# Performance work log

Measured on AMD Instinct MI355X. Metric: run time of the kernel, lower is better.

## Reference

```python
import jax, jax.numpy as jnp
import numpy as np

N = 32767      # 2**15 - 1 nodes: complete binary tree, parent(i) = (i-1)//2
IN = 512       # in_channels
H = 256        # hidden_dim
OUT = 1        # output_dim
DEPTH = 15     # number of topological levels (static)


def setup_inputs() -> dict:
    key = jax.random.key(0)
    ks = jax.random.split(key, 8)
    x = jax.random.normal(ks[0], (N, IN), dtype=jnp.float32)
    # complete binary tree edge list: edge_index[0]=child, edge_index[1]=parent
    src = jnp.arange(1, N, dtype=jnp.int32)
    dst = (src - 1) // 2
    edge_index = jnp.stack([src, dst])  # [2, N-1]
    s = 1.0 / np.sqrt(H)  # torch LSTMCell/Linear default uniform init scale
    W_ih = jax.random.uniform(ks[1], (4 * H, IN), minval=-s, maxval=s, dtype=jnp.float32)
    W_hh = jax.random.uniform(ks[2], (4 * H, H), minval=-s, maxval=s, dtype=jnp.float32)
    b_ih = jax.random.uniform(ks[3], (4 * H,), minval=-s, maxval=s, dtype=jnp.float32)
    b_hh = jax.random.uniform(ks[4], (4 * H,), minval=-s, maxval=s, dtype=jnp.float32)
    W_fc = jax.random.uniform(ks[5], (OUT, H), minval=-s, maxval=s, dtype=jnp.float32)
    b_fc = jax.random.uniform(ks[6], (OUT,), minval=-s, maxval=s, dtype=jnp.float32)
    return {"x": x, "edge_index": edge_index, "W_ih": W_ih, "W_hh": W_hh,
            "b_ih": b_ih, "b_hh": b_hh, "W_fc": W_fc, "b_fc": b_fc}


def reference(x, edge_index, W_ih, W_hh, b_ih, b_hh, W_fc, b_fc):
    src, dst = edge_index[0], edge_index[1]
    # children count per parent (matches torch children_count loop)
    cnt = jax.ops.segment_sum(jnp.ones_like(src, dtype=x.dtype), dst, num_segments=N)
    cnt = jnp.maximum(cnt, 1.0)[:, None]  # [N,1]; leaves get zero child state anyway
    h = jnp.zeros((N, H), dtype=x.dtype)
    c = jnp.zeros((N, H), dtype=x.dtype)
    # topological sweep: deepest level first (children processed before parents)
    for d in range(DEPTH - 1, -1, -1):
        lo = 2 ** d - 1
        hi = min(2 ** (d + 1) - 1, N)  # level d node index range (static)
        # mean of already-computed child h/c states, gathered via edge list
        mean_h = jax.ops.segment_sum(h[src], dst, num_segments=N)[lo:hi] / cnt[lo:hi]
        mean_c = jax.ops.segment_sum(c[src], dst, num_segments=N)[lo:hi] / cnt[lo:hi]
        # torch LSTMCell: gates in (i, f, g, o) order
        gates = x[lo:hi] @ W_ih.T + b_ih + mean_h @ W_hh.T + b_hh  # [n_level, 4H]
        i, f, g, o = jnp.split(gates, 4, axis=-1)
        i, f, o = jax.nn.sigmoid(i), jax.nn.sigmoid(f), jax.nn.sigmoid(o)
        g = jnp.tanh(g)
        c_new = f * mean_c + i * g
        h_new = o * jnp.tanh(c_new)
        h = h.at[lo:hi].set(h_new)
        c = c.at[lo:hi].set(c_new)
    pooled = jnp.mean(h, axis=0, keepdims=True)  # [1, H]
    out = pooled @ W_fc.T + b_fc                 # [1, 1]
    return out.squeeze(-1)                       # [1]
```

## Files before the change

### kernel.cpp

```cpp
#include <hip/hip_runtime.h>
#include <hip/hip_cooperative_groups.h>
#include <math.h>

namespace cg = cooperative_groups;


#define N_NODES 32767
#define N_LEAF0 16383
#define IN_C    512
#define H_C     256

typedef __bf16 bf16x8 __attribute__((ext_vector_type(8)));
typedef float  f32x4  __attribute__((ext_vector_type(4)));

__device__ __forceinline__ void gload_lds16(const void* g, void* l) {
    __builtin_amdgcn_global_load_lds(
        (const __attribute__((address_space(1))) unsigned int*)g,
        (__attribute__((address_space(3))) unsigned int*)l,
        16, 0, 0);
}

__device__ __forceinline__ float fast_rcp(float x) { return __builtin_amdgcn_rcpf(x); }
__device__ __forceinline__ float sigm(float x)     { return fast_rcp(1.f + __expf(-x)); }
__device__ __forceinline__ float tanh_fast(float x){ return 2.f * fast_rcp(1.f + __expf(-2.f * x)) - 1.f; }

__global__ __launch_bounds__(256)
void conv_bf16_kernel(const float* __restrict__ src, __bf16* __restrict__ dst, int n8)
{
    const int i = blockIdx.x * 256 + threadIdx.x;
    if (i < n8) {
        const float4* s4 = (const float4*)src;
        const float4 a = s4[2 * i];
        const float4 b = s4[2 * i + 1];
        bf16x8 o;
        o[0] = (__bf16)a.x; o[1] = (__bf16)a.y; o[2] = (__bf16)a.z; o[3] = (__bf16)a.w;
        o[4] = (__bf16)b.x; o[5] = (__bf16)b.y; o[6] = (__bf16)b.z; o[7] = (__bf16)b.w;
        *(bf16x8*)(dst + 8 * i) = o;
    }
}

__global__ __launch_bounds__(256)
void bulk_xw(const float* __restrict__ x,
             const __bf16* __restrict__ wih,
             const float* __restrict__ b_ih,
             const float* __restrict__ b_hh,
             __bf16* __restrict__ hb,
             float* __restrict__ c,
             __bf16* __restrict__ gx)
{
    __shared__ __bf16 As[128 * 64];
    __shared__ __bf16 Bs[128 * 64];

    const int t    = threadIdx.x;
    const int lane = t & 63;
    const int wv   = t >> 6;
    const int wm   = wv >> 1;
    const int wn   = wv & 1;
    const int quad = lane >> 4;
    const int l15  = lane & 15;

    const int i  = blockIdx.x;
    const int cb = (i >> 3) & 7;
    const int mt = (i & 7) | ((i >> 6) << 3);
    const int m0 = mt * 128;

    f32x4 acc[4][4];
#pragma unroll
    for (int mi = 0; mi < 4; ++mi)
#pragma unroll
        for (int ni = 0; ni < 4; ++ni) acc[mi][ni] = (f32x4)0.f;

    for (int k0 = 0; k0 < IN_C; k0 += 64) {
#pragma unroll
        for (int e = 0; e < 4; ++e) {
            const int ch = (wv * 4 + e) * 64 + lane;
            const int nl = ch >> 3;
            const int k8 = (ch & 7) ^ (nl & 7);
            const int q  = (nl >> 4) & 3;
            const int cc = (nl & 15) | ((nl >> 6) << 4);
            const int grow = q * H_C + cb * 32 + cc;
            gload_lds16(wih + (size_t)grow * IN_C + k0 + k8 * 8,
                        (char*)Bs + (wv * 4 + e) * 1024);
        }
        {
            const int row  = t >> 1;
            const int kh   = (t & 1) * 32;
            const int node = min(m0 + row, N_NODES - 1);
            const float4* xs = (const float4*)(x + (size_t)node * IN_C + k0 + kh);
#pragma unroll
            for (int j = 0; j < 4; ++j) {
                const float4 v0 = xs[2 * j], v1 = xs[2 * j + 1];
                bf16x8 o;
                o[0] = (__bf16)v0.x; o[1] = (__bf16)v0.y; o[2] = (__bf16)v0.z; o[3] = (__bf16)v0.w;
                o[4] = (__bf16)v1.x; o[5] = (__bf16)v1.y; o[6] = (__bf16)v1.z; o[7] = (__bf16)v1.w;
                const int cs = ((kh >> 3) + j) ^ (row & 7);
                *(bf16x8*)(As + row * 64 + cs * 8) = o;
            }
        }
        __syncthreads();
#pragma unroll
        for (int ks = 0; ks < 2; ++ks) {
            bf16x8 af[4], bfr[4];
#pragma unroll
            for (int mi = 0; mi < 4; ++mi) {
                const int row = wm * 64 + mi * 16 + l15;
                af[mi] = *(const bf16x8*)(As + row * 64 + (((ks * 4 + quad) ^ (row & 7)) << 3));
            }
#pragma unroll
            for (int ni = 0; ni < 4; ++ni) {
                const int row = wn * 64 + ni * 16 + l15;
                bfr[ni] = *(const bf16x8*)(Bs + row * 64 + (((ks * 4 + quad) ^ (row & 7)) << 3));
            }
#pragma unroll
            for (int mi = 0; mi < 4; ++mi)
#pragma unroll
                for (int ni = 0; ni < 4; ++ni)
                    acc[mi][ni] = __builtin_amdgcn_mfma_f32_16x16x32_bf16(
                        af[mi], bfr[ni], acc[mi][ni], 0, 0, 0);
        }
        __syncthreads();
    }

    const int CH = cb * 32 + wn * 16 + l15;
    float bs[4];
#pragma unroll
    for (int q = 0; q < 4; ++q) bs[q] = b_ih[q * H_C + CH] + b_hh[q * H_C + CH];

#pragma unroll
    for (int mi = 0; mi < 4; ++mi) {
#pragma unroll
        for (int r = 0; r < 4; ++r) {
            const int m = m0 + wm * 64 + mi * 16 + quad * 4 + r;
            if (m >= N_NODES) continue;
            if (m >= N_LEAF0) {
                const float gi = sigm(acc[mi][0][r] + bs[0]);
                const float gf = sigm(acc[mi][1][r] + bs[1]);  (void)gf;
                const float gg = tanh_fast(acc[mi][2][r] + bs[2]);
                const float go = sigm(acc[mi][3][r] + bs[3]);
                const float cn = gi * gg;
                const float hn = go * tanh_fast(cn);
                c[(size_t)m * H_C + CH] = cn;
                hb[(size_t)m * H_C + CH] = (__bf16)hn;
            } else {
#pragma unroll
                for (int q = 0; q < 4; ++q)
                    gx[(size_t)m * 1024 + q * H_C + CH] = (__bf16)acc[mi][q][r];
            }
        }
    }
}

__global__ __launch_bounds__(256)
void level_hw(const __bf16* __restrict__ whh,
              const float* __restrict__ b_ih,
              const float* __restrict__ b_hh,
              const __bf16* __restrict__ gx,
              __bf16* __restrict__ hb,
              float* __restrict__ c,
              int lo, int n)
{
    __shared__ __bf16 As[128 * 32];
    __shared__ __bf16 Bs[128 * 32];

    const int t    = threadIdx.x;
    const int lane = t & 63;
    const int wv   = t >> 6;
    const int wm   = wv >> 1;
    const int wn   = wv & 1;
    const int quad = lane >> 4;
    const int l15  = lane & 15;

    const int i = blockIdx.x;
    int cb, mt;
    if (gridDim.x >= 64) { cb = (i >> 3) & 7; mt = (i & 7) | ((i >> 6) << 3); }
    else                 { cb = i & 7;        mt = i >> 3; }
    const int m0 = mt * 128;

    f32x4 acc[4][4];
#pragma unroll
    for (int mi = 0; mi < 4; ++mi)
#pragma unroll
        for (int ni = 0; ni < 4; ++ni) acc[mi][ni] = (f32x4)0.f;

    for (int k0 = 0; k0 < H_C; k0 += 32) {
#pragma unroll
        for (int e = 0; e < 2; ++e) {
            const int chunk = wv * 2 + e;
            const int nl    = chunk * 16 + (lane >> 2);
            const int q     = (nl >> 4) & 3;
            const int cc    = (nl & 15) + ((nl >> 6) << 4);
            const int grow  = q * H_C + cb * 32 + cc;
            const void* g = (const char*)(whh + grow * H_C + k0) + (lane & 3) * 16;
            gload_lds16(g, (char*)Bs + chunk * 1024);
        }
        {
            const int row  = t >> 1;
            const int kh   = (t & 1) * 16;
            const int node = lo + m0 + row;
            const int k2   = k0 + kh;
            const bf16x8* hl = (const bf16x8*)(hb + (size_t)(2 * node + 1) * H_C + k2);
            const bf16x8* hr = (const bf16x8*)(hb + (size_t)(2 * node + 2) * H_C + k2);
            const bf16x8 a0 = hl[0], a1 = hl[1], b0 = hr[0], b1 = hr[1];
            bf16x8 o0, o1;
#pragma unroll
            for (int j = 0; j < 8; ++j) {
                o0[j] = (__bf16)(0.5f * ((float)a0[j] + (float)b0[j]));
                o1[j] = (__bf16)(0.5f * ((float)a1[j] + (float)b1[j]));
            }
            bf16x8* dst = (bf16x8*)(As + row * 32 + kh);
            dst[0] = o0;
            dst[1] = o1;
        }
        __syncthreads();
        bf16x8 af[4], bfr[4];
#pragma unroll
        for (int mi = 0; mi < 4; ++mi)
            af[mi] = *(const bf16x8*)(As + (wm * 64 + mi * 16 + l15) * 32 + quad * 8);
#pragma unroll
        for (int ni = 0; ni < 4; ++ni)
            bfr[ni] = *(const bf16x8*)(Bs + (wn * 64 + ni * 16 + l15) * 32 + quad * 8);
#pragma unroll
        for (int mi = 0; mi < 4; ++mi)
#pragma unroll
            for (int ni = 0; ni < 4; ++ni)
                acc[mi][ni] = __builtin_amdgcn_mfma_f32_16x16x32_bf16(
                    af[mi], bfr[ni], acc[mi][ni], 0, 0, 0);
        __syncthreads();
    }

    const int CH = cb * 32 + wn * 16 + l15;
    float bs[4];
#pragma unroll
    for (int q = 0; q < 4; ++q) bs[q] = b_ih[q * H_C + CH] + b_hh[q * H_C + CH];

#pragma unroll
    for (int mi = 0; mi < 4; ++mi) {
#pragma unroll
        for (int r = 0; r < 4; ++r) {
            const int m = m0 + wm * 64 + mi * 16 + quad * 4 + r;
            if (m < n) {
                const int node = lo + m;
                const float g0 = acc[mi][0][r] + (float)gx[(size_t)node * 1024 + 0 * H_C + CH] + bs[0];
                const float g1 = acc[mi][1][r] + (float)gx[(size_t)node * 1024 + 1 * H_C + CH] + bs[1];
                const float g2 = acc[mi][2][r] + (float)gx[(size_t)node * 1024 + 2 * H_C + CH] + bs[2];
                const float g3 = acc[mi][3][r] + (float)gx[(size_t)node * 1024 + 3 * H_C + CH] + bs[3];
                const float gi = sigm(g0);
                const float gf = sigm(g1);
                const float gg = tanh_fast(g2);
                const float go = sigm(g3);
                const float mc = 0.5f * (c[(size_t)(2 * node + 1) * H_C + CH] +
                                         c[(size_t)(2 * node + 2) * H_C + CH]);
                const float cn = gf * mc + gi * gg;
                const float hn = go * tanh_fast(cn);
                c[(size_t)node * H_C + CH] = cn;
                hb[(size_t)node * H_C + CH] = (__bf16)hn;
            }
        }
    }
}

__global__ __launch_bounds__(256, 1)
void tail_levels(const __bf16* __restrict__ whh,
                 const float* __restrict__ b_ih,
                 const float* __restrict__ b_hh,
                 const __bf16* __restrict__ gx,
                 __bf16* __restrict__ hb,
                 const float* __restrict__ c)
{
    __shared__ __bf16 Ws[128][264];
    __shared__ __align__(16) char UAG[64 * 264 * 2];
    __shared__ float cl[2][64][33];

    const int t    = threadIdx.x;
    const int cb   = blockIdx.x;
    const int lane = t & 63;
    const int wq   = t >> 6;
    const int quad = lane >> 4;
    const int l15  = lane & 15;

    auto As = (__bf16(*)[264])UAG;
    auto Gs = (float(*)[64][33])UAG;

    {
        const int row = t >> 1;
        const int k0  = (t & 1) * 128;
        const int q   = row >> 5, cc = row & 31;
        const __bf16* src = whh + (size_t)(q * H_C + cb * 32 + cc) * H_C + k0;
#pragma unroll
        for (int j = 0; j < 16; ++j)
            *(bf16x8*)(&Ws[row][k0 + 8 * j]) = *(const bf16x8*)(src + 8 * j);
    }
    const int ecc = t & 31;
    const int erg = t >> 5;
    const int CH  = cb * 32 + ecc;
    float bsq[4];
#pragma unroll
    for (int q = 0; q < 4; ++q) bsq[q] = b_ih[q * H_C + CH] + b_hh[q * H_C + CH];

    cg::grid_group grid = cg::this_grid();

    for (int d = 6; d >= 0; --d) {
        const int n  = 1 << d;
        const int lo = n - 1;
        const int pp = d & 1;
        __syncthreads();
        {
            const int row  = t >> 2;
            const int kb   = (t & 3) * 64;
            const int node = lo + row;
            const bf16x8* hl = (const bf16x8*)(hb + (size_t)(2 * node + 1) * H_C + kb);
            const bf16x8* hr = (const bf16x8*)(hb + (size_t)(2 * node + 2) * H_C + kb);
#pragma unroll
            for (int j = 0; j < 8; ++j) {
                const bf16x8 a = hl[j], b = hr[j];
                bf16x8 o;
#pragma unroll
                for (int e = 0; e < 8; ++e)
                    o[e] = (__bf16)(0.5f * ((float)a[e] + (float)b[e]));
                *(bf16x8*)(&As[row][kb + 8 * j]) = o;
            }
        }
        __syncthreads();
        f32x4 acc[4][2];
#pragma unroll
        for (int mi = 0; mi < 4; ++mi)
#pragma unroll
            for (int ni = 0; ni < 2; ++ni) acc[mi][ni] = (f32x4)0.f;
        for (int kk = 0; kk < 8; ++kk) {
#pragma unroll
            for (int mi = 0; mi < 4; ++mi) {
                const bf16x8 af = *(const bf16x8*)(&As[mi * 16 + l15][kk * 32 + quad * 8]);
#pragma unroll
                for (int ni = 0; ni < 2; ++ni) {
                    const bf16x8 bf_ = *(const bf16x8*)(&Ws[wq * 32 + ni * 16 + l15][kk * 32 + quad * 8]);
                    acc[mi][ni] = __builtin_amdgcn_mfma_f32_16x16x32_bf16(af, bf_, acc[mi][ni], 0, 0, 0);
                }
            }
        }
        __syncthreads();
#pragma unroll
        for (int mi = 0; mi < 4; ++mi)
#pragma unroll
            for (int ni = 0; ni < 2; ++ni)
#pragma unroll
                for (int r = 0; r < 4; ++r)
                    Gs[wq][mi * 16 + quad * 4 + r][ni * 16 + l15] = acc[mi][ni][r];
        __syncthreads();
        for (int r = erg; r < n; r += 8) {
            const int node = lo + r;
            float g[4];
#pragma unroll
            for (int q = 0; q < 4; ++q)
                g[q] = Gs[q][r][ecc] + (float)gx[(size_t)node * 1024 + q * H_C + CH] + bsq[q];
            const float gi = sigm(g[0]);
            const float gf = sigm(g[1]);
            const float gg = tanh_fast(g[2]);
            const float go = sigm(g[3]);
            float mc;
            if (d == 6)
                mc = 0.5f * (c[(size_t)(2 * node + 1) * H_C + CH] +
                             c[(size_t)(2 * node + 2) * H_C + CH]);
            else
                mc = 0.5f * (cl[pp ^ 1][2 * r][ecc] + cl[pp ^ 1][2 * r + 1][ecc]);
            const float cn = gf * mc + gi * gg;
            const float hn = go * tanh_fast(cn);
            cl[pp][r][ecc] = cn;
            hb[(size_t)node * H_C + CH] = (__bf16)hn;
        }
        grid.sync();
    }
}

__global__ __launch_bounds__(256)
void reduce_rows(const __bf16* __restrict__ hb, float* __restrict__ part)
{
    __shared__ float sm[8][256];
    const int t  = threadIdx.x;
    const int b  = blockIdx.x;
    const int rg = t >> 5;
    const int c8 = (t & 31) * 8;
    float s[8];
#pragma unroll
    for (int j = 0; j < 8; ++j) s[j] = 0.f;
    for (int i2 = 0; i2 < 16; ++i2) {
        const int row = b * 128 + i2 * 8 + rg;
        if (row < N_NODES) {
            const bf16x8 v = *(const bf16x8*)(hb + (size_t)row * H_C + c8);
#pragma unroll
            for (int j = 0; j < 8; ++j) s[j] += (float)v[j];
        }
    }
#pragma unroll
    for (int j = 0; j < 8; ++j) sm[rg][c8 + j] = s[j];
    __syncthreads();
    float tot = 0.f;
#pragma unroll
    for (int g = 0; g < 8; ++g) tot += sm[g][t];
    part[b * H_C + t] = tot;
}

__global__ __launch_bounds__(256)
void reduce_final(const float* __restrict__ part,
                  const float* __restrict__ W_fc,
                  const float* __restrict__ b_fc,
                  float* __restrict__ out)
{
    __shared__ float sm[256];
    const int t = threadIdx.x;
    float s = 0.f;
    for (int j = 0; j < 256; ++j) s += part[j * H_C + t];
    s = s * (1.0f / (float)N_NODES) * W_fc[t];
    sm[t] = s;
    __syncthreads();
    for (int st = 128; st > 0; st >>= 1) {
        if (t < st) sm[t] += sm[t + st];
        __syncthreads();
    }
    if (t == 0) out[0] = sm[0] + b_fc[0];
}

extern "C" void kernel_launch(void* const* d_in, const int* in_sizes, int n_in,
                              void* d_out, int out_size, void* d_ws, size_t ws_size,
                              hipStream_t stream)
{
    const float* x    = (const float*)d_in[0];
    const float* W_ih = (const float*)d_in[2];
    const float* W_hh = (const float*)d_in[3];
    const float* b_ih = (const float*)d_in[4];
    const float* b_hh = (const float*)d_in[5];
    const float* W_fc = (const float*)d_in[6];
    const float* b_fc = (const float*)d_in[7];
    float* out = (float*)d_out;

    char* w = (char*)d_ws;
    __bf16* hb   = (__bf16*)w;  w += (size_t)N_NODES * H_C * 2;
    float*  c    = (float*)w;   w += (size_t)N_NODES * H_C * 4;
    __bf16* gx   = (__bf16*)w;  w += (size_t)N_LEAF0 * 1024 * 2;
    __bf16* wihb = (__bf16*)w;  w += (size_t)4 * H_C * IN_C * 2;
    __bf16* whhb = (__bf16*)w;  w += (size_t)4 * H_C * H_C * 2;
    float*  part = (float*)w;

    {
        const int n8i = (4 * H_C * IN_C) / 8;
        conv_bf16_kernel<<<(n8i + 255) / 256, 256, 0, stream>>>(W_ih, wihb, n8i);
        const int n8h = (4 * H_C * H_C) / 8;
        conv_bf16_kernel<<<(n8h + 255) / 256, 256, 0, stream>>>(W_hh, whhb, n8h);
    }

    bulk_xw<<<2048, 256, 0, stream>>>(x, wihb, b_ih, b_hh, hb, c, gx);

    for (int d = 13; d >= 7; --d) {
        const int n  = 1 << d;
        const int lo = n - 1;
        const int nm = (n + 127) / 128;
        level_hw<<<nm * 8, 256, 0, stream>>>(whhb, b_ih, b_hh, gx, hb, c, lo, n);
    }

    {
        const __bf16* a0 = whhb; const float* a1 = b_ih; const float* a2 = b_hh;
        const __bf16* a3 = gx;   __bf16* a4 = hb;        const float* a5 = c;
        void* targs[] = {&a0, &a1, &a2, &a3, &a4, &a5};
        hipError_t e = hipLaunchCooperativeKernel((const void*)tail_levels,
                                                  dim3(8), dim3(256), targs, 0, stream);
        if (e != hipSuccess) {
            for (int d = 6; d >= 0; --d) {
                const int n  = 1 << d;
                const int lo = n - 1;
                level_hw<<<8, 256, 0, stream>>>(whhb, b_ih, b_hh, gx, hb, c, lo, n);
            }
        }
    }

    reduce_rows<<<256, 256, 0, stream>>>(hb, part);
    reduce_final<<<1, 256, 0, stream>>>(part, W_fc, b_fc, out);
}
```

Measured before the change: 422.1 us.

## Fuse pooling into level kernels, merge weight casts, extend cooperative tail to more levels

Several changes at once. The two weight-conversion kernels are merged into one grid-stride launch. The x loads in bulk_xw are register-prefetched one k-step ahead. The gx layout is interleaved so each node/channel reads one 8-byte vector. level_hw gets a larger K tile with a swizzled LDS layout. The mean-pool is fused into every stage through atomic per-channel sums, which removes the two reduction kernels. The cooperative 8-block tail now covers levels 9..0 in 64-row chunks, replacing three more launches but doing more serial work on only 8 blocks.

```diff
diff --git a/kernel.cpp b/kernel.cpp
--- a/kernel.cpp
+++ b/kernel.cpp
@@ -11,6 +11,7 @@
 #define H_C     256
 
 typedef __bf16 bf16x8 __attribute__((ext_vector_type(8)));
+typedef __bf16 bf16x4 __attribute__((ext_vector_type(4)));
 typedef float  f32x4  __attribute__((ext_vector_type(4)));
 
 __device__ __forceinline__ void gload_lds16(const void* g, void* l) {
@@ -25,17 +26,23 @@
 __device__ __forceinline__ float tanh_fast(float x){ return 2.f * fast_rcp(1.f + __expf(-2.f * x)) - 1.f; }
 
 __global__ __launch_bounds__(256)
-void conv_bf16_kernel(const float* __restrict__ src, __bf16* __restrict__ dst, int n8)
-{
-    const int i = blockIdx.x * 256 + threadIdx.x;
-    if (i < n8) {
-        const float4* s4 = (const float4*)src;
-        const float4 a = s4[2 * i];
-        const float4 b = s4[2 * i + 1];
+void conv2(const float* __restrict__ a, __bf16* __restrict__ da, int n8a,
+           const float* __restrict__ b, __bf16* __restrict__ db, int n8b,
+           float* __restrict__ hsum)
+{
+    if (blockIdx.x == 0 && threadIdx.x < 256) hsum[threadIdx.x] = 0.f;
+    const int total = n8a + n8b;
+    for (int i = blockIdx.x * 256 + threadIdx.x; i < total; i += gridDim.x * 256) {
+        const float* s; __bf16* d; int j;
+        if (i < n8a) { s = a; d = da; j = i; }
+        else         { s = b; d = db; j = i - n8a; }
+        const float4* s4 = (const float4*)s;
+        const float4 v0 = s4[2 * j];
+        const float4 v1 = s4[2 * j + 1];
         bf16x8 o;
-        o[0] = (__bf16)a.x; o[1] = (__bf16)a.y; o[2] = (__bf16)a.z; o[3] = (__bf16)a.w;
-        o[4] = (__bf16)b.x; o[5] = (__bf16)b.y; o[6] = (__bf16)b.z; o[7] = (__bf16)b.w;
-        *(bf16x8*)(dst + 8 * i) = o;
+        o[0] = (__bf16)v0.x; o[1] = (__bf16)v0.y; o[2] = (__bf16)v0.z; o[3] = (__bf16)v0.w;
+        o[4] = (__bf16)v1.x; o[5] = (__bf16)v1.y; o[6] = (__bf16)v1.z; o[7] = (__bf16)v1.w;
+        *(bf16x8*)(d + 8 * j) = o;
     }
 }
 
@@ -46,10 +53,12 @@
              const float* __restrict__ b_hh,
              __bf16* __restrict__ hb,
              float* __restrict__ c,
-             __bf16* __restrict__ gx)
+             __bf16* __restrict__ gx,
+             float* __restrict__ hsum)
 {
     __shared__ __bf16 As[128 * 64];
     __shared__ __bf16 Bs[128 * 64];
+    __shared__ float  hs[32];
 
     const int t    = threadIdx.x;
     const int lane = t & 63;
@@ -59,6 +68,8 @@
     const int quad = lane >> 4;
     const int l15  = lane & 15;
 
+    if (t < 32) hs[t] = 0.f;
+
     const int i  = blockIdx.x;
     const int cb = (i >> 3) & 7;
     const int mt = (i & 7) | ((i >> 6) << 3);
@@ -69,6 +80,14 @@
     for (int mi = 0; mi < 4; ++mi)
 #pragma unroll
         for (int ni = 0; ni < 4; ++ni) acc[mi][ni] = (f32x4)0.f;
+
+    const int arow = t >> 1;
+    const int kh   = (t & 1) * 32;
+    const int anode = min(m0 + arow, N_NODES - 1);
+    const float* xrow = x + (size_t)anode * IN_C + kh;
+    float4 xr[8];
+#pragma unroll
+    for (int j = 0; j < 8; ++j) xr[j] = ((const float4*)xrow)[j];
 
     for (int k0 = 0; k0 < IN_C; k0 += 64) {
 #pragma unroll
@@ -82,22 +101,21 @@
             gload_lds16(wih + (size_t)grow * IN_C + k0 + k8 * 8,
                         (char*)Bs + (wv * 4 + e) * 1024);
         }
-        {
-            const int row  = t >> 1;
-            const int kh   = (t & 1) * 32;
-            const int node = min(m0 + row, N_NODES - 1);
-            const float4* xs = (const float4*)(x + (size_t)node * IN_C + k0 + kh);
-#pragma unroll
-            for (int j = 0; j < 4; ++j) {
-                const float4 v0 = xs[2 * j], v1 = xs[2 * j + 1];
-                bf16x8 o;
-                o[0] = (__bf16)v0.x; o[1] = (__bf16)v0.y; o[2] = (__bf16)v0.z; o[3] = (__bf16)v0.w;
-                o[4] = (__bf16)v1.x; o[5] = (__bf16)v1.y; o[6] = (__bf16)v1.z; o[7] = (__bf16)v1.w;
-                const int cs = ((kh >> 3) + j) ^ (row & 7);
-                *(bf16x8*)(As + row * 64 + cs * 8) = o;
-            }
+#pragma unroll
+        for (int j = 0; j < 4; ++j) {
+            const float4 v0 = xr[2 * j], v1 = xr[2 * j + 1];
+            bf16x8 o;
+            o[0] = (__bf16)v0.x; o[1] = (__bf16)v0.y; o[2] = (__bf16)v0.z; o[3] = (__bf16)v0.w;
+            o[4] = (__bf16)v1.x; o[5] = (__bf16)v1.y; o[6] = (__bf16)v1.z; o[7] = (__bf16)v1.w;
+            const int cs = ((kh >> 3) + j) ^ (arow & 7);
+            *(bf16x8*)(As + arow * 64 + cs * 8) = o;
         }
         __syncthreads();
+        if (k0 + 64 < IN_C) {
+            const float4* xs = (const float4*)(xrow + k0 + 64);
+#pragma unroll
+            for (int j = 0; j < 8; ++j) xr[j] = xs[j];
+        }
 #pragma unroll
         for (int ks = 0; ks < 2; ++ks) {
             bf16x8 af[4], bfr[4];
@@ -122,10 +140,11 @@
     }
 
     const int CH = cb * 32 + wn * 16 + l15;
-    float bs[4];
-#pragma unroll
-    for (int q = 0; q < 4; ++q) bs[q] = b_ih[q * H_C + CH] + b_hh[q * H_C + CH];
-
+    float bs4[4];
+#pragma unroll
+    for (int q = 0; q < 4; ++q) bs4[q] = b_ih[q * H_C + CH] + b_hh[q * H_C + CH];
+
+    float lh = 0.f;
 #pragma unroll
     for (int mi = 0; mi < 4; ++mi) {
 #pragma unroll
@@ -133,21 +152,132 @@
             const int m = m0 + wm * 64 + mi * 16 + quad * 4 + r;
             if (m >= N_NODES) continue;
             if (m >= N_LEAF0) {
-                const float gi = sigm(acc[mi][0][r] + bs[0]);
-                const float gf = sigm(acc[mi][1][r] + bs[1]);  (void)gf;
-                const float gg = tanh_fast(acc[mi][2][r] + bs[2]);
-                const float go = sigm(acc[mi][3][r] + bs[3]);
+                const float gi = sigm(acc[mi][0][r] + bs4[0]);
+                const float gg = tanh_fast(acc[mi][2][r] + bs4[2]);
+                const float go = sigm(acc[mi][3][r] + bs4[3]);
                 const float cn = gi * gg;
                 const float hn = go * tanh_fast(cn);
                 c[(size_t)m * H_C + CH] = cn;
                 hb[(size_t)m * H_C + CH] = (__bf16)hn;
+                lh += hn;
             } else {
-#pragma unroll
-                for (int q = 0; q < 4; ++q)
-                    gx[(size_t)m * 1024 + q * H_C + CH] = (__bf16)acc[mi][q][r];
-            }
-        }
-    }
+                bf16x4 o;
+#pragma unroll
+                for (int q = 0; q < 4; ++q) o[q] = (__bf16)acc[mi][q][r];
+                *(bf16x4*)(gx + ((size_t)m * H_C + CH) * 4) = o;
+            }
+        }
+    }
+    atomicAdd(&hs[wn * 16 + l15], lh);
+    __syncthreads();
+    if (t < 32) atomicAdd(&hsum[cb * 32 + t], hs[t]);
+}
+
+__device__ __forceinline__ void level_tile(
+    const __bf16* __restrict__ whh, const float* __restrict__ b_ih,
+    const float* __restrict__ b_hh, const __bf16* __restrict__ gx,
+    __bf16* __restrict__ hb, float* __restrict__ c, float* __restrict__ hsum,
+    __bf16* As, __bf16* Bs, float* hs, int lo, int n, int cb, int m0)
+{
+    const int t    = threadIdx.x;
+    const int lane = t & 63;
+    const int wv   = t >> 6;
+    const int wm   = wv >> 1;
+    const int wn   = wv & 1;
+    const int quad = lane >> 4;
+    const int l15  = lane & 15;
+
+    f32x4 acc[4][4];
+#pragma unroll
+    for (int mi = 0; mi < 4; ++mi)
+#pragma unroll
+        for (int ni = 0; ni < 4; ++ni) acc[mi][ni] = (f32x4)0.f;
+
+    for (int k0 = 0; k0 < H_C; k0 += 64) {
+#pragma unroll
+        for (int e = 0; e < 4; ++e) {
+            const int ch = (wv * 4 + e) * 64 + lane;
+            const int nl = ch >> 3;
+            const int k8 = (ch & 7) ^ (nl & 7);
+            const int q  = (nl >> 4) & 3;
+            const int cc = (nl & 15) | ((nl >> 6) << 4);
+            const int grow = q * H_C + cb * 32 + cc;
+            gload_lds16(whh + (size_t)grow * H_C + k0 + k8 * 8,
+                        (char*)Bs + (wv * 4 + e) * 1024);
+        }
+        {
+            const int row  = t >> 1;
+            const int kh   = (t & 1) * 32;
+            const int node = lo + m0 + row;
+            const int k2   = k0 + kh;
+            const bf16x8* hl = (const bf16x8*)(hb + (size_t)(2 * node + 1) * H_C + k2);
+            const bf16x8* hr = (const bf16x8*)(hb + (size_t)(2 * node + 2) * H_C + k2);
+#pragma unroll
+            for (int j = 0; j < 4; ++j) {
+                const bf16x8 a = hl[j], b = hr[j];
+                bf16x8 o;
+#pragma unroll
+                for (int e2 = 0; e2 < 8; ++e2)
+                    o[e2] = (__bf16)(0.5f * ((float)a[e2] + (float)b[e2]));
+                const int cs = ((kh >> 3) + j) ^ (row & 7);
+                *(bf16x8*)(As + row * 64 + cs * 8) = o;
+            }
+        }
+        __syncthreads();
+#pragma unroll
+        for (int ks = 0; ks < 2; ++ks) {
+            bf16x8 af[4], bfr[4];
+#pragma unroll
+            for (int mi = 0; mi < 4; ++mi) {
+                const int row = wm * 64 + mi * 16 + l15;
+                af[mi] = *(const bf16x8*)(As + row * 64 + (((ks * 4 + quad) ^ (row & 7)) << 3));
+            }
+#pragma unroll
+            for (int ni = 0; ni < 4; ++ni) {
+                const int row = wn * 64 + ni * 16 + l15;
+                bfr[ni] = *(const bf16x8*)(Bs + row * 64 + (((ks * 4 + quad) ^ (row & 7)) << 3));
+            }
+#pragma unroll
+            for (int mi = 0; mi < 4; ++mi)
+#pragma unroll
+                for (int ni = 0; ni < 4; ++ni)
+                    acc[mi][ni] = __builtin_amdgcn_mfma_f32_16x16x32_bf16(
+                        af[mi], bfr[ni], acc[mi][ni], 0, 0, 0);
+        }
+        __syncthreads();
+    }
+
+    const int CH = cb * 32 + wn * 16 + l15;
+    float bs4[4];
+#pragma unroll
+    for (int q = 0; q < 4; ++q) bs4[q] = b_ih[q * H_C + CH] + b_hh[q * H_C + CH];
+
+    float lh = 0.f;
+#pragma unroll
+    for (int mi = 0; mi < 4; ++mi) {
+#pragma unroll
+        for (int r = 0; r < 4; ++r) {
+            const int m = m0 + wm * 64 + mi * 16 + quad * 4 + r;
+            if (m < n) {
+                const int node = lo + m;
+                const bf16x4 gv = *(const bf16x4*)(gx + ((size_t)node * H_C + CH) * 4);
+                const float gi = sigm(acc[mi][0][r] + (float)gv[0] + bs4[0]);
+                const float gf = sigm(acc[mi][1][r] + (float)gv[1] + bs4[1]);
+                const float gg = tanh_fast(acc[mi][2][r] + (float)gv[2] + bs4[2]);
+                const float go = sigm(acc[mi][3][r] + (float)gv[3] + bs4[3]);
+                const float mc = 0.5f * (c[(size_t)(2 * node + 1) * H_C + CH] +
+                                         c[(size_t)(2 * node + 2) * H_C + CH]);
+                const float cn = gf * mc + gi * gg;
+                const float hn = go * tanh_fast(cn);
+                c[(size_t)node * H_C + CH] = cn;
+                hb[(size_t)node * H_C + CH] = (__bf16)hn;
+                lh += hn;
+            }
+        }
+    }
+    atomicAdd(&hs[wn * 16 + l15], lh);
+    __syncthreads();
+    if (t < 32) atomicAdd(&hsum[cb * 32 + t], hs[t]);
 }
 
 __global__ __launch_bounds__(256)
@@ -157,106 +287,18 @@
               const __bf16* __restrict__ gx,
               __bf16* __restrict__ hb,
               float* __restrict__ c,
+              float* __restrict__ hsum,
               int lo, int n)
 {
-    __shared__ __bf16 As[128 * 32];
-    __shared__ __bf16 Bs[128 * 32];
-
-    const int t    = threadIdx.x;
-    const int lane = t & 63;
-    const int wv   = t >> 6;
-    const int wm   = wv >> 1;
-    const int wn   = wv & 1;
-    const int quad = lane >> 4;
-    const int l15  = lane & 15;
-
+    __shared__ __bf16 As[128 * 64];
+    __shared__ __bf16 Bs[128 * 64];
+    __shared__ float  hs[32];
+    if (threadIdx.x < 32) hs[threadIdx.x] = 0.f;
     const int i = blockIdx.x;
     int cb, mt;
     if (gridDim.x >= 64) { cb = (i >> 3) & 7; mt = (i & 7) | ((i >> 6) << 3); }
     else                 { cb = i & 7;        mt = i >> 3; }
-    const int m0 = mt * 128;
-
-    f32x4 acc[4][4];
-#pragma unroll
-    for (int mi = 0; mi < 4; ++mi)
-#pragma unroll
-        for (int ni = 0; ni < 4; ++ni) acc[mi][ni] = (f32x4)0.f;
-
-    for (int k0 = 0; k0 < H_C; k0 += 32) {
-#pragma unroll
-        for (int e = 0; e < 2; ++e) {
-            const int chunk = wv * 2 + e;
-            const int nl    = chunk * 16 + (lane >> 2);
-            const int q     = (nl >> 4) & 3;
-            const int cc    = (nl & 15) + ((nl >> 6) << 4);
-            const int grow  = q * H_C + cb * 32 + cc;
-            const void* g = (const char*)(whh + grow * H_C + k0) + (lane & 3) * 16;
-            gload_lds16(g, (char*)Bs + chunk * 1024);
-        }
-        {
-            const int row  = t >> 1;
-            const int kh   = (t & 1) * 16;
-            const int node = lo + m0 + row;
-            const int k2   = k0 + kh;
-            const bf16x8* hl = (const bf16x8*)(hb + (size_t)(2 * node + 1) * H_C + k2);
-            const bf16x8* hr = (const bf16x8*)(hb + (size_t)(2 * node + 2) * H_C + k2);
-            const bf16x8 a0 = hl[0], a1 = hl[1], b0 = hr[0], b1 = hr[1];
-            bf16x8 o0, o1;
-#pragma unroll
-            for (int j = 0; j < 8; ++j) {
-                o0[j] = (__bf16)(0.5f * ((float)a0[j] + (float)b0[j]));
-                o1[j] = (__bf16)(0.5f * ((float)a1[j] + (float)b1[j]));
-            }
-            bf16x8* dst = (bf16x8*)(As + row * 32 + kh);
-            dst[0] = o0;
-            dst[1] = o1;
-        }
-        __syncthreads();
-        bf16x8 af[4], bfr[4];
-#pragma unroll
-        for (int mi = 0; mi < 4; ++mi)
-            af[mi] = *(const bf16x8*)(As + (wm * 64 + mi * 16 + l15) * 32 + quad * 8);
-#pragma unroll
-        for (int ni = 0; ni < 4; ++ni)
-            bfr[ni] = *(const bf16x8*)(Bs + (wn * 64 + ni * 16 + l15) * 32 + quad * 8);
-#pragma unroll
-        for (int mi = 0; mi < 4; ++mi)
-#pragma unroll
-            for (int ni = 0; ni < 4; ++ni)
-                acc[mi][ni] = __builtin_amdgcn_mfma_f32_16x16x32_bf16(
-                    af[mi], bfr[ni], acc[mi][ni], 0, 0, 0);
-        __syncthreads();
-    }
-
-    const int CH = cb * 32 + wn * 16 + l15;
-    float bs[4];
-#pragma unroll
-    for (int q = 0; q < 4; ++q) bs[q] = b_ih[q * H_C + CH] + b_hh[q * H_C + CH];
-
-#pragma unroll
-    for (int mi = 0; mi < 4; ++mi) {
-#pragma unroll
-        for (int r = 0; r < 4; ++r) {
-            const int m = m0 + wm * 64 + mi * 16 + quad * 4 + r;
-            if (m < n) {
-                const int node = lo + m;
-                const float g0 = acc[mi][0][r] + (float)gx[(size_t)node * 1024 + 0 * H_C + CH] + bs[0];
-                const float g1 = acc[mi][1][r] + (float)gx[(size_t)node * 1024 + 1 * H_C + CH] + bs[1];
-                const float g2 = acc[mi][2][r] + (float)gx[(size_t)node * 1024 + 2 * H_C + CH] + bs[2];
-                const float g3 = acc[mi][3][r] + (float)gx[(size_t)node * 1024 + 3 * H_C + CH] + bs[3];
-                const float gi = sigm(g0);
-                const float gf = sigm(g1);
-                const float gg = tanh_fast(g2);
-                const float go = sigm(g3);
-                const float mc = 0.5f * (c[(size_t)(2 * node + 1) * H_C + CH] +
-                                         c[(size_t)(2 * node + 2) * H_C + CH]);
-                const float cn = gf * mc + gi * gg;
-                const float hn = go * tanh_fast(cn);
-                c[(size_t)node * H_C + CH] = cn;
-                hb[(size_t)node * H_C + CH] = (__bf16)hn;
-            }
-        }
-    }
+    level_tile(whh, b_ih, b_hh, gx, hb, c, hsum, As, Bs, hs, lo, n, cb, mt * 128);
 }
 
 __global__ __launch_bounds__(256, 1)
@@ -265,11 +307,17 @@
                  const float* __restrict__ b_hh,
                  const __bf16* __restrict__ gx,
                  __bf16* __restrict__ hb,
-                 const float* __restrict__ c)
+                 float* __restrict__ c,
+                 float* __restrict__ hsum,
+                 const float* __restrict__ W_fc,
+                 const float* __restrict__ b_fc,
+                 float* __restrict__ out)
 {
     __shared__ __bf16 Ws[128][264];
     __shared__ __align__(16) char UAG[64 * 264 * 2];
     __shared__ float cl[2][64][33];
+    __shared__ float hs[32];
+    __shared__ float fm[256];
 
     const int t    = threadIdx.x;
     const int cb   = blockIdx.x;
@@ -281,6 +329,8 @@
     auto As = (__bf16(*)[264])UAG;
     auto Gs = (float(*)[64][33])UAG;
 
+    if (t < 32) hs[t] = 0.f;
+
     {
         const int row = t >> 1;
         const int k0  = (t & 1) * 128;
@@ -296,127 +346,120 @@
     float bsq[4];
 #pragma unroll
     for (int q = 0; q < 4; ++q) bsq[q] = b_ih[q * H_C + CH] + b_hh[q * H_C + CH];
+    float th = 0.f;
 
     cg::grid_group grid = cg::this_grid();
 
-    for (int d = 6; d >= 0; --d) {
-        const int n  = 1 << d;
-        const int lo = n - 1;
-        const int pp = d & 1;
+    for (int d = 9; d >= 0; --d) {
+        const int n   = 1 << d;
+        const int lo  = n - 1;
+        const int pp  = d & 1;
+        const int nck = (n + 63) >> 6;
+        for (int ck = 0; ck < nck; ++ck) {
+            const int rbase = ck * 64;
+            const int rows  = (n - rbase < 64) ? (n - rbase) : 64;
+            __syncthreads();
+            {
+                const int row  = t >> 2;
+                const int kb   = (t & 3) * 64;
+                const int node = lo + rbase + row;
+                const bf16x8* hl = (const bf16x8*)(hb + (size_t)(2 * node + 1) * H_C + kb);
+                const bf16x8* hr = (const bf16x8*)(hb + (size_t)(2 * node + 2) * H_C + kb);
+#pragma unroll
+                for (int j = 0; j < 8; ++j) {
+                    const bf16x8 a = hl[j], b = hr[j];
+                    bf16x8 o;
+#pragma unroll
+                    for (int e = 0; e < 8; ++e)
+                        o[e] = (__bf16)(0.5f * ((float)a[e] + (float)b[e]));
+                    *(bf16x8*)(&As[row][kb + 8 * j]) = o;
+                }
+            }
+            __syncthreads();
+            f32x4 acc[4][2];
+#pragma unroll
+            for (int mi = 0; mi < 4; ++mi)
+#pragma unroll
+                for (int ni = 0; ni < 2; ++ni) acc[mi][ni] = (f32x4)0.f;
+            for (int kk = 0; kk < 8; ++kk) {
+#pragma unroll
+                for (int mi = 0; mi < 4; ++mi) {
+                    const bf16x8 af = *(const bf16x8*)(&As[mi * 16 + l15][kk * 32 + quad * 8]);
+#pragma unroll
+                    for (int ni = 0; ni < 2; ++ni) {
+                        const bf16x8 bf_ = *(const bf16x8*)(&Ws[wq * 32 + ni * 16 + l15][kk * 32 + quad * 8]);
+                        acc[mi][ni] = __builtin_amdgcn_mfma_f32_16x16x32_bf16(af, bf_, acc[mi][ni], 0, 0, 0);
+                    }
+                }
+            }
+            __syncthreads();
+#pragma unroll
+            for (int mi = 0; mi < 4; ++mi)
+#pragma unroll
+                for (int ni = 0; ni < 2; ++ni)
+#pragma unroll
+                    for (int r = 0; r < 4; ++r)
+                        Gs[wq][mi * 16 + quad * 4 + r][ni * 16 + l15] = acc[mi][ni][r];
+            __syncthreads();
+            for (int r = erg; r < rows; r += 8) {
+                const int rr   = rbase + r;
+                const int node = lo + rr;
+                const bf16x4 gv = *(const bf16x4*)(gx + ((size_t)node * H_C + CH) * 4);
+                float g[4];
+#pragma unroll
+                for (int q = 0; q < 4; ++q) g[q] = Gs[q][r][ecc] + (float)gv[q] + bsq[q];
+                const float gi = sigm(g[0]);
+                const float gf = sigm(g[1]);
+                const float gg = tanh_fast(g[2]);
+                const float go = sigm(g[3]);
+                float mc;
+                if (d >= 6)
+                    mc = 0.5f * (c[(size_t)(2 * node + 1) * H_C + CH] +
+                                 c[(size_t)(2 * node + 2) * H_C + CH]);
+                else
+                    mc = 0.5f * (cl[pp ^ 1][2 * rr][ecc] + cl[pp ^ 1][2 * rr + 1][ecc]);
+                const float cn = gf * mc + gi * gg;
+                const float hn = go * tanh_fast(cn);
+                if (d >= 7) c[(size_t)node * H_C + CH] = cn;
+                else        cl[pp][rr][ecc] = cn;
+                hb[(size_t)node * H_C + CH] = (__bf16)hn;
+                th += hn;
+            }
+        }
+        grid.sync();
+    }
+
+    atomicAdd(&hs[ecc], th);
+    __syncthreads();
+    if (t < 32) atomicAdd(&hsum[cb * 32 + t], hs[t]);
+    grid.sync();
+
+    if (cb == 0) {
+        fm[t] = hsum[t] * (1.0f / (float)N_NODES) * W_fc[t];
         __syncthreads();
-        {
-            const int row  = t >> 2;
-            const int kb   = (t & 3) * 64;
-            const int node = lo + row;
-            const bf16x8* hl = (const bf16x8*)(hb + (size_t)(2 * node + 1) * H_C + kb);
-            const bf16x8* hr = (const bf16x8*)(hb + (size_t)(2 * node + 2) * H_C + kb);
-#pragma unroll
-            for (int j = 0; j < 8; ++j) {
-                const bf16x8 a = hl[j], b = hr[j];
-                bf16x8 o;
-#pragma unroll
-                for (int e = 0; e < 8; ++e)
-                    o[e] = (__bf16)(0.5f * ((float)a[e] + (float)b[e]));
-                *(bf16x8*)(&As[row][kb + 8 * j]) = o;
-            }
-        }
-        __syncthreads();
-        f32x4 acc[4][2];
-#pragma unroll
-        for (int mi = 0; mi < 4; ++mi)
-#pragma unroll
-            for (int ni = 0; ni < 2; ++ni) acc[mi][ni] = (f32x4)0.f;
-        for (int kk = 0; kk < 8; ++kk) {
-#pragma unroll
-            for (int mi = 0; mi < 4; ++mi) {
-                const bf16x8 af = *(const bf16x8*)(&As[mi * 16 + l15][kk * 32 + quad * 8]);
-#pragma unroll
-                for (int ni = 0; ni < 2; ++ni) {
-                    const bf16x8 bf_ = *(const bf16x8*)(&Ws[wq * 32 + ni * 16 + l15][kk * 32 + quad * 8]);
-                    acc[mi][ni] = __builtin_amdgcn_mfma_f32_16x16x32_bf16(af, bf_, acc[mi][ni], 0, 0, 0);
-                }
-            }
-        }
-        __syncthreads();
-#pragma unroll
-        for (int mi = 0; mi < 4; ++mi)
-#pragma unroll
-            for (int ni = 0; ni < 2; ++ni)
-#pragma unroll
-                for (int r = 0; r < 4; ++r)
-                    Gs[wq][mi * 16 + quad * 4 + r][ni * 16 + l15] = acc[mi][ni][r];
-        __syncthreads();
-        for (int r = erg; r < n; r += 8) {
-            const int node = lo + r;
-            float g[4];
-#pragma unroll
-            for (int q = 0; q < 4; ++q)
-                g[q] = Gs[q][r][ecc] + (float)gx[(size_t)node * 1024 + q * H_C + CH] + bsq[q];
-            const float gi = sigm(g[0]);
-            const float gf = sigm(g[1]);
-            const float gg = tanh_fast(g[2]);
-            const float go = sigm(g[3]);
-            float mc;
-            if (d == 6)
-                mc = 0.5f * (c[(size_t)(2 * node + 1) * H_C + CH] +
-                             c[(size_t)(2 * node + 2) * H_C + CH]);
-            else
-                mc = 0.5f * (cl[pp ^ 1][2 * r][ecc] + cl[pp ^ 1][2 * r + 1][ecc]);
-            const float cn = gf * mc + gi * gg;
-            const float hn = go * tanh_fast(cn);
-            cl[pp][r][ecc] = cn;
-            hb[(size_t)node * H_C + CH] = (__bf16)hn;
-        }
-        grid.sync();
+        for (int st = 128; st > 0; st >>= 1) {
+            if (t < st) fm[t] += fm[t + st];
+            __syncthreads();
+        }
+        if (t == 0) out[0] = fm[0] + b_fc[0];
     }
 }
 
 __global__ __launch_bounds__(256)
-void reduce_rows(const __bf16* __restrict__ hb, float* __restrict__ part)
-{
-    __shared__ float sm[8][256];
-    const int t  = threadIdx.x;
-    const int b  = blockIdx.x;
-    const int rg = t >> 5;
-    const int c8 = (t & 31) * 8;
-    float s[8];
-#pragma unroll
-    for (int j = 0; j < 8; ++j) s[j] = 0.f;
-    for (int i2 = 0; i2 < 16; ++i2) {
-        const int row = b * 128 + i2 * 8 + rg;
-        if (row < N_NODES) {
-            const bf16x8 v = *(const bf16x8*)(hb + (size_t)row * H_C + c8);
-#pragma unroll
-            for (int j = 0; j < 8; ++j) s[j] += (float)v[j];
-        }
-    }
-#pragma unroll
-    for (int j = 0; j < 8; ++j) sm[rg][c8 + j] = s[j];
-    __syncthreads();
-    float tot = 0.f;
-#pragma unroll
-    for (int g = 0; g < 8; ++g) tot += sm[g][t];
-    part[b * H_C + t] = tot;
-}
-
-__global__ __launch_bounds__(256)
-void reduce_final(const float* __restrict__ part,
-                  const float* __restrict__ W_fc,
-                  const float* __restrict__ b_fc,
-                  float* __restrict__ out)
-{
-    __shared__ float sm[256];
+void final_out(const float* __restrict__ hsum,
+               const float* __restrict__ W_fc,
+               const float* __restrict__ b_fc,
+               float* __restrict__ out)
+{
+    __shared__ float fm[256];
     const int t = threadIdx.x;
-    float s = 0.f;
-    for (int j = 0; j < 256; ++j) s += part[j * H_C + t];
-    s = s * (1.0f / (float)N_NODES) * W_fc[t];
-    sm[t] = s;
+    fm[t] = hsum[t] * (1.0f / (float)N_NODES) * W_fc[t];
     __syncthreads();
     for (int st = 128; st > 0; st >>= 1) {
-        if (t < st) sm[t] += sm[t + st];
+        if (t < st) fm[t] += fm[t + st];
         __syncthreads();
     }
-    if (t == 0) out[0] = sm[0] + b_fc[0];
+    if (t == 0) out[0] = fm[0] + b_fc[0];
 }
 
 extern "C" void kernel_launch(void* const* d_in, const int* in_sizes, int n_in,
@@ -433,44 +476,45 @@
     float* out = (float*)d_out;
 
     char* w = (char*)d_ws;
-    __bf16* hb   = (__bf16*)w;  w += (size_t)N_NODES * H_C * 2;
-    float*  c    = (float*)w;   w += (size_t)N_NODES * H_C * 4;
-    __bf16* gx   = (__bf16*)w;  w += (size_t)N_LEAF0 * 1024 * 2;
-    __bf16* wihb = (__bf16*)w;  w += (size_t)4 * H_C * IN_C * 2;
-    __bf16* whhb = (__bf16*)w;  w += (size_t)4 * H_C * H_C * 2;
-    float*  part = (float*)w;
+    size_t used = 0;
+    __bf16* hb   = (__bf16*)(w + used); used += (size_t)N_NODES * H_C * 2;
+    float*  c    = (float*)(w + used);  used += (size_t)N_NODES * H_C * 4;
+    __bf16* gx   = (__bf16*)(w + used); used += (size_t)N_LEAF0 * H_C * 4 * 2;
+    __bf16* wihb = (__bf16*)(w + used); used += (size_t)4 * H_C * IN_C * 2;
+    __bf16* whhb = (__bf16*)(w + used); used += (size_t)4 * H_C * H_C * 2;
+    float*  hsum = (float*)(w + used);  used += 256 * 4;
 
     {
         const int n8i = (4 * H_C * IN_C) / 8;
-        conv_bf16_kernel<<<(n8i + 255) / 256, 256, 0, stream>>>(W_ih, wihb, n8i);
         const int n8h = (4 * H_C * H_C) / 8;
-        conv_bf16_kernel<<<(n8h + 255) / 256, 256, 0, stream>>>(W_hh, whhb, n8h);
-    }
-
-    bulk_xw<<<2048, 256, 0, stream>>>(x, wihb, b_ih, b_hh, hb, c, gx);
-
-    for (int d = 13; d >= 7; --d) {
+        conv2<<<384, 256, 0, stream>>>(W_ih, wihb, n8i, W_hh, whhb, n8h, hsum);
+    }
+
+    bulk_xw<<<2048, 256, 0, stream>>>(x, wihb, b_ih, b_hh, hb, c, gx, hsum);
+
+    for (int d = 13; d >= 10; --d) {
         const int n  = 1 << d;
         const int lo = n - 1;
         const int nm = (n + 127) / 128;
-        level_hw<<<nm * 8, 256, 0, stream>>>(whhb, b_ih, b_hh, gx, hb, c, lo, n);
+        level_hw<<<nm * 8, 256, 0, stream>>>(whhb, b_ih, b_hh, gx, hb, c, hsum, lo, n);
     }
 
     {
         const __bf16* a0 = whhb; const float* a1 = b_ih; const float* a2 = b_hh;
-        const __bf16* a3 = gx;   __bf16* a4 = hb;        const float* a5 = c;
-        void* targs[] = {&a0, &a1, &a2, &a3, &a4, &a5};
+        const __bf16* a3 = gx;   __bf16* a4 = hb;        float* a5 = c;
+        float* a6 = hsum;        const float* a7 = W_fc; const float* a8 = b_fc;
+        float* a9 = out;
+        void* targs[] = {&a0, &a1, &a2, &a3, &a4, &a5, &a6, &a7, &a8, &a9};
         hipError_t e = hipLaunchCooperativeKernel((const void*)tail_levels,
                                                   dim3(8), dim3(256), targs, 0, stream);
         if (e != hipSuccess) {
-            for (int d = 6; d >= 0; --d) {
+            for (int d = 9; d >= 0; --d) {
                 const int n  = 1 << d;
                 const int lo = n - 1;
-                level_hw<<<8, 256, 0, stream>>>(whhb, b_ih, b_hh, gx, hb, c, lo, n);
-            }
-        }
-    }
-
-    reduce_rows<<<256, 256, 0, stream>>>(hb, part);
-    reduce_final<<<1, 256, 0, stream>>>(part, W_fc, b_fc, out);
-}
+                const int nm = (n + 127) / 128;
+                level_hw<<<nm * 8, 256, 0, stream>>>(whhb, b_ih, b_hh, gx, hb, c, hsum, lo, n);
+            }
+            final_out<<<1, 256, 0, stream>>>(hsum, W_fc, b_fc, out);
+        }
+    }
+}
```

After: 465.3 us. 1.1x slower.
